# Optimization experiments

Measured on AMD Instinct MI355X. Metric: run time of the kernel, lower is better.

Reference implementation:

```python
import jax, jax.numpy as jnp
import numpy as np

EPS = 1e-8

def squash(t, axis=-1):
    sq = jnp.sum(t * t, axis=axis, keepdims=True)
    scale = sq / (1.0 + sq)
    return scale * t / jnp.sqrt(sq + EPS)

def setup_inputs() -> dict:
    key = jax.random.key(0)
    k1, k2 = jax.random.split(key)
    B, N_IN, D_IN, N_OUT, D_OUT = 256, 1152, 8, 10, 16
    x = jax.random.normal(k1, (B, N_IN, D_IN), dtype=jnp.float32)
    W = 0.01 * jax.random.normal(k2, (1, N_IN, N_OUT, D_OUT, D_IN), dtype=jnp.float32)
    return {"x": x, "W": W}

def reference(x, W):
    # u_hat[b,n,o,j] = sum_i W[0,n,o,j,i] * x[b,n,i]   -> (B, N_in, N_out, D_out)
    u_hat = jnp.einsum('noji,bni->bnoj', W[0], x)
    # b_ij starts with batch dim 1 (as in original torch code) and broadcasts
    b_ij = jnp.zeros((1, u_hat.shape[1], u_hat.shape[2], 1), dtype=u_hat.dtype)
    v_j = None
    for _ in range(3):  # fixed 3 routing iterations
        c_ij = jax.nn.softmax(b_ij, axis=2)            # over output capsules
        s_j = jnp.sum(c_ij * u_hat, axis=1, keepdims=True)  # (B,1,N_out,D_out)
        v_j = squash(s_j, axis=-1)
        b_ij = b_ij + jnp.sum(u_hat * v_j, axis=-1, keepdims=True)
    return jnp.squeeze(v_j, axis=1)  # (B, N_out, D_out)
```

## Files before the change

kernel.cpp:

```cpp
#include <hip/hip_runtime.h>

#define B_ 256
#define N_IN 1152
#define N_OUT 10
#define D_OUT 16
#define OJ 160
#define SN (B_*OJ)
#define LOG2E 1.44269504088896340736f
#define NPB 16
#define NPW 4
#define NSG (N_IN/NPB)
#define NPASSB (NSG*16)
#define NPB1 32
#define NSG1 (N_IN/NPB1)

typedef __attribute__((ext_vector_type(8))) short bf16x8;
typedef __attribute__((ext_vector_type(4))) float f32x4;

#define NW_ELEMS (N_IN*N_OUT*D_OUT)
#define NX_ELEMS (B_*N_IN)
#define NWB (NW_ELEMS/256)
#define NTILES ((N_IN/16)*(B_/16))

__device__ __forceinline__ unsigned short f2bf(float f) {
  unsigned u = __float_as_uint(f);
  u += 0x7fffu + ((u >> 16) & 1u);
  return (unsigned short)(u >> 16);
}
__device__ __forceinline__ float bf2f(unsigned short s) {
  return __uint_as_float(((unsigned)s) << 16);
}
__device__ __forceinline__ void split8(const float* p, bf16x8& vh, bf16x8& vl) {
  const float4 a = *(const float4*)p;
  const float4 b = *(const float4*)(p + 4);
  const float w[8] = {a.x,a.y,a.z,a.w,b.x,b.y,b.z,b.w};
#pragma unroll
  for (int e=0;e<8;e++){
    unsigned short hh = f2bf(w[e]);
    vh[e] = (short)hh;
    vl[e] = (short)f2bf(w[e] - bf2f(hh));
  }
}

template<int CTRL>
__device__ __forceinline__ float dpp_add(float xx) {
  int y = __builtin_amdgcn_mov_dpp(__float_as_int(xx), CTRL, 0xF, 0xF, false);
  return xx + __int_as_float(y);
}
__device__ __forceinline__ float quad_sum4(float xx) {
  xx = dpp_add<0xB1>(xx);
  xx = dpp_add<0x4E>(xx);
  return xx;
}

__device__ __forceinline__ void sgbg_map(int bid, int& sg, int& bg) {
  const int xcd = bid & 7, q = bid >> 3;
  sg = xcd*9 + (q % 9);
  bg = q / 9;
}

__global__ __launch_bounds__(256) void pack_all(const float* __restrict__ W,
                                                const float* __restrict__ x,
                                                short* __restrict__ WH, short* __restrict__ WL,
                                                short* __restrict__ XH, short* __restrict__ XL) {
  const int bid = blockIdx.x, tid = threadIdx.x;
  if (bid < NWB) {
    const int t = bid*256 + tid;
    bf16x8 vh, vl; split8(W + (size_t)t*8, vh, vl);
    ((bf16x8*)WH)[t] = vh; ((bf16x8*)WL)[t] = vl;
  } else {
    __shared__ bf16x8 TH[16*17], TL[16*17];
    const int tile = bid - NWB;
    const int nt = tile >> 4, bt = tile & 15;
    const int nn = tid & 15, bb = tid >> 4;
    bf16x8 vh, vl;
    split8(x + ((size_t)(bt*16+bb)*N_IN + nt*16+nn)*8, vh, vl);
    TH[nn*17 + bb] = vh; TL[nn*17 + bb] = vl;
    __syncthreads();
    const int bb2 = tid & 15, nn2 = tid >> 4;
    const size_t o = (size_t)(nt*16+nn2)*B_ + bt*16 + bb2;
    ((bf16x8*)XH)[o] = TH[nn2*17 + bb2];
    ((bf16x8*)XL)[o] = TL[nn2*17 + bb2];
  }
}

__global__ __launch_bounds__(256) void caps_pass1(const short* __restrict__ WH,
                                                  const short* __restrict__ XH,
                                                  float* __restrict__ P) {
  __shared__ f32x4 red[3*640];
  const int tid = threadIdx.x, w = tid >> 6, l = tid & 63;
  const int bb = l & 15, c = l >> 4;
  const int sg = blockIdx.x, bg = blockIdx.y;
  const int b0 = bg * 16;
  const int n0 = sg*NPB1 + w*8;

  f32x4 acc[N_OUT];
  const f32x4 zz = {0.f,0.f,0.f,0.f};
#pragma unroll
  for (int o=0;o<N_OUT;o++) acc[o] = zz;

#pragma unroll
  for (int grp=0; grp<2; ++grp) {
    const int nb = n0 + grp*4 + c;
    const bf16x8 bfrag = *(const bf16x8*)&XH[((size_t)nb*B_ + b0 + bb)*8];
    const short* Ap = &WH[(size_t)nb*1280 + bb*8];
#pragma unroll
    for (int o=0;o<N_OUT;o++) {
      const bf16x8 afrag = *(const bf16x8*)&Ap[o*128];
      acc[o] = __builtin_amdgcn_mfma_f32_16x16x32_bf16(afrag, bfrag, acc[o], 0,0,0);
    }
  }

  if (w) {
#pragma unroll
    for (int o=0;o<N_OUT;o++) red[(w-1)*640 + o*64 + l] = acc[o];
  }
  __syncthreads();
  if (!w) {
    float* Pp = &P[(size_t)sg*SN + (size_t)(b0 + bb)*OJ + c*4];
#pragma unroll
    for (int o=0;o<N_OUT;o++) {
      acc[o] += red[o*64+l] + red[640+o*64+l] + red[1280+o*64+l];
      *(f32x4*)&Pp[o*16] = acc[o];
    }
  }
}

__global__ __launch_bounds__(256) void caps_pass23(const short* __restrict__ WH,
                                                   const short* __restrict__ WL,
                                                   const short* __restrict__ XH,
                                                   const short* __restrict__ XL,
                                                   const float* __restrict__ veff,
                                                   float* __restrict__ P) {
  __shared__ f32x4 red[3*640];
  int sg, bg; sgbg_map(blockIdx.x, sg, bg);
  const int tid = threadIdx.x, w = tid >> 6, l = tid & 63;
  const int bb = l & 15, c = l >> 4;
  const int b0 = bg * 16;
  const int n0 = sg * NPB + w * NPW;
  const short* Abase = (c & 1)  ? WL : WH;
  const short* Bbase = (c >> 1) ? XL : XH;

  f32x4 vj[N_OUT], acc[N_OUT];
  const f32x4 zz = {0.f,0.f,0.f,0.f};
  const float* vp = &veff[(size_t)(b0+bb)*OJ + c*4];
#pragma unroll
  for (int o=0;o<N_OUT;o++) { vj[o] = *(const f32x4*)&vp[o*16]; acc[o] = zz; }

  for (int nn=0; nn<NPW; ++nn) {
    const int n = n0 + nn;
    const bf16x8 bfrag = *(const bf16x8*)&Bbase[((size_t)n*B_ + b0 + bb)*8];
    const short* Ap = &Abase[(size_t)n*1280 + bb*8];
    f32x4 u[N_OUT];
#pragma unroll
    for (int o=0;o<N_OUT;o++) {
      const bf16x8 afrag = *(const bf16x8*)&Ap[o*128];
      u[o] = __builtin_amdgcn_mfma_f32_16x16x32_bf16(afrag, bfrag, zz, 0,0,0);
    }
    float ez[N_OUT], Z = 0.f;
#pragma unroll
    for (int o=0;o<N_OUT;o++) {
      float t = u[o][0]*vj[o][0] + u[o][1]*vj[o][1]
              + u[o][2]*vj[o][2] + u[o][3]*vj[o][3];
      t += __shfl_xor(t, 16);
      t += __shfl_xor(t, 32);
      ez[o] = exp2f(t);
      Z += ez[o];
    }
    const float invZ = __builtin_amdgcn_rcpf(Z);
#pragma unroll
    for (int o=0;o<N_OUT;o++) acc[o] += (ez[o] * invZ) * u[o];
  }

  if (w) {
#pragma unroll
    for (int o=0;o<N_OUT;o++) red[(w-1)*640 + o*64 + l] = acc[o];
  }
  __syncthreads();
  if (!w) {
    float* Pp = &P[(size_t)sg*SN + (size_t)(b0 + bb)*OJ + c*4];
#pragma unroll
    for (int o=0;o<N_OUT;o++) {
      acc[o] += red[o*64+l] + red[640+o*64+l] + red[1280+o*64+l];
      *(f32x4*)&Pp[o*16] = acc[o];
    }
  }
}

template<int GC>
__global__ __launch_bounds__(256) void caps_finish(const float* __restrict__ P, float scale,
                                                   const float* __restrict__ vprev,
                                                   float* __restrict__ vout, float lscale) {
  const int e0 = (blockIdx.x*256 + threadIdx.x)*4;
  f32x4 t = {0.f,0.f,0.f,0.f};
#pragma unroll 8
  for (int g=0; g<GC; ++g) t += *(const f32x4*)&P[(size_t)g*SN + e0];
  t *= scale;
  const float sq = quad_sum4(t[0]*t[0] + t[1]*t[1] + t[2]*t[2] + t[3]*t[3]);
  const float k = (sq/(1.f+sq)) * rsqrtf(sq + 1e-8f) * lscale;
  f32x4 v = t * k;
  if (vprev != nullptr) v += *(const f32x4*)&vprev[e0];
  *(f32x4*)&vout[e0] = v;
}

extern "C" void kernel_launch(void* const* d_in, const int* in_sizes, int n_in,
                              void* d_out, int out_size, void* d_ws, size_t ws_size,
                              hipStream_t stream) {
  const float* x = (const float*)d_in[0];
  const float* W = (const float*)d_in[1];
  float* out = (float*)d_out;

  float* P   = (float*)d_ws;
  float* v1  = P  + (size_t)NSG*SN;
  float* v12 = v1 + SN;
  short* WH = (short*)(v12 + SN);
  short* WL = WH + (size_t)NW_ELEMS*8;
  short* XH = WL + (size_t)NW_ELEMS*8;
  short* XL = XH + (size_t)NX_ELEMS*8;

  pack_all<<<NWB + NTILES, 256, 0, stream>>>(W, x, WH, WL, XH, XL);

  caps_pass1<<<dim3(NSG1,16), 256, 0, stream>>>(WH, XH, P);
  caps_finish<NSG1><<<SN/1024, 256, 0, stream>>>(P, 0.1f, nullptr, v1, LOG2E);

  caps_pass23<<<NPASSB, 256, 0, stream>>>(WH, WL, XH, XL, v1, P);
  caps_finish<NSG><<<SN/1024, 256, 0, stream>>>(P, 1.0f, v1, v12, LOG2E);

  caps_pass23<<<NPASSB, 256, 0, stream>>>(WH, WL, XH, XL, v12, P);
  caps_finish<NSG><<<SN/1024, 256, 0, stream>>>(P, 1.0f, nullptr, out, 1.0f);
}
```

Measured before the change: 79.44 us.

## Fuse first routing pass into pack kernel, converting fp32 inputs to bf16 on the fly

The separate pack and pass-1 kernels are merged into one launch. Pass-1 blocks now read fp32 W and x directly and convert them to bf16 with v_cvt_pk_bf16_f32, so they no longer wait for the packed buffers. This removes one kernel launch and the serial dependency between packing and the first pass. In exchange, pass-1 reads W and x twice from global memory and uses the hardware conversion's rounding rather than the software round-to-nearest-even.

```diff
diff --git a/kernel.cpp b/kernel.cpp
--- a/kernel.cpp
+++ b/kernel.cpp
@@ -13,6 +13,7 @@
 #define NPASSB (NSG*16)
 #define NPB1 32
 #define NSG1 (N_IN/NPB1)
+#define NP1B (NSG1*16)
 
 typedef __attribute__((ext_vector_type(8))) short bf16x8;
 typedef __attribute__((ext_vector_type(4))) float f32x4;
@@ -42,6 +43,17 @@
   }
 }
 
+__device__ __forceinline__ bf16x8 cvt8(const float* p) {
+  const f32x4 a = *(const f32x4*)p;
+  const f32x4 b = *(const f32x4*)(p + 4);
+  union { unsigned u[4]; bf16x8 v; } r;
+  asm("v_cvt_pk_bf16_f32 %0, %1, %2" : "=v"(r.u[0]) : "v"(a[0]), "v"(a[1]));
+  asm("v_cvt_pk_bf16_f32 %0, %1, %2" : "=v"(r.u[1]) : "v"(a[2]), "v"(a[3]));
+  asm("v_cvt_pk_bf16_f32 %0, %1, %2" : "=v"(r.u[2]) : "v"(b[0]), "v"(b[1]));
+  asm("v_cvt_pk_bf16_f32 %0, %1, %2" : "=v"(r.u[3]) : "v"(b[2]), "v"(b[3]));
+  return r.v;
+}
+
 template<int CTRL>
 __device__ __forceinline__ float dpp_add(float xx) {
   int y = __builtin_amdgcn_mov_dpp(__float_as_int(xx), CTRL, 0xF, 0xF, false);
@@ -59,18 +71,59 @@
   bg = q / 9;
 }
 
-__global__ __launch_bounds__(256) void pack_all(const float* __restrict__ W,
-                                                const float* __restrict__ x,
-                                                short* __restrict__ WH, short* __restrict__ WL,
-                                                short* __restrict__ XH, short* __restrict__ XL) {
+__global__ __launch_bounds__(256) void d1_all(
+    const float* __restrict__ W, const float* __restrict__ x,
+    short* __restrict__ WH, short* __restrict__ WL,
+    short* __restrict__ XH, short* __restrict__ XL,
+    float* __restrict__ P) {
+  __shared__ f32x4 red[3*640];
   const int bid = blockIdx.x, tid = threadIdx.x;
-  if (bid < NWB) {
-    const int t = bid*256 + tid;
+
+  if (bid < NP1B) {
+    const int sg = bid >> 4, bg = bid & 15;
+    const int w = tid >> 6, l = tid & 63;
+    const int bb = l & 15, c = l >> 4;
+    const int b0 = bg * 16;
+    const int n0 = sg*NPB1 + w*8;
+
+    f32x4 acc[N_OUT];
+    const f32x4 zz = {0.f,0.f,0.f,0.f};
+#pragma unroll
+    for (int o=0;o<N_OUT;o++) acc[o] = zz;
+
+#pragma unroll
+    for (int grp=0; grp<2; ++grp) {
+      const int nb = n0 + grp*4 + c;
+      const bf16x8 bfrag = cvt8(&x[((size_t)(b0+bb)*N_IN + nb)*8]);
+      const float* Wp = &W[(size_t)nb*1280 + bb*8];
+#pragma unroll
+      for (int o=0;o<N_OUT;o++) {
+        const bf16x8 afrag = cvt8(Wp + o*128);
+        acc[o] = __builtin_amdgcn_mfma_f32_16x16x32_bf16(afrag, bfrag, acc[o], 0,0,0);
+      }
+    }
+
+    if (w) {
+#pragma unroll
+      for (int o=0;o<N_OUT;o++) red[(w-1)*640 + o*64 + l] = acc[o];
+    }
+    __syncthreads();
+    if (!w) {
+      float* Pp = &P[(size_t)sg*SN + (size_t)(b0 + bb)*OJ + c*4];
+#pragma unroll
+      for (int o=0;o<N_OUT;o++) {
+        acc[o] += red[o*64+l] + red[640+o*64+l] + red[1280+o*64+l];
+        *(f32x4*)&Pp[o*16] = acc[o];
+      }
+    }
+  } else if (bid < NP1B + NWB) {
+    const int t = (bid - NP1B)*256 + tid;
     bf16x8 vh, vl; split8(W + (size_t)t*8, vh, vl);
     ((bf16x8*)WH)[t] = vh; ((bf16x8*)WL)[t] = vl;
   } else {
-    __shared__ bf16x8 TH[16*17], TL[16*17];
-    const int tile = bid - NWB;
+    bf16x8* TH = (bf16x8*)red;
+    bf16x8* TL = TH + 272;
+    const int tile = bid - NP1B - NWB;
     const int nt = tile >> 4, bt = tile & 15;
     const int nn = tid & 15, bb = tid >> 4;
     bf16x8 vh, vl;
@@ -81,48 +134,6 @@
     const size_t o = (size_t)(nt*16+nn2)*B_ + bt*16 + bb2;
     ((bf16x8*)XH)[o] = TH[nn2*17 + bb2];
     ((bf16x8*)XL)[o] = TL[nn2*17 + bb2];
-  }
-}
-
-__global__ __launch_bounds__(256) void caps_pass1(const short* __restrict__ WH,
-                                                  const short* __restrict__ XH,
-                                                  float* __restrict__ P) {
-  __shared__ f32x4 red[3*640];
-  const int tid = threadIdx.x, w = tid >> 6, l = tid & 63;
-  const int bb = l & 15, c = l >> 4;
-  const int sg = blockIdx.x, bg = blockIdx.y;
-  const int b0 = bg * 16;
-  const int n0 = sg*NPB1 + w*8;
-
-  f32x4 acc[N_OUT];
-  const f32x4 zz = {0.f,0.f,0.f,0.f};
-#pragma unroll
-  for (int o=0;o<N_OUT;o++) acc[o] = zz;
-
-#pragma unroll
-  for (int grp=0; grp<2; ++grp) {
-    const int nb = n0 + grp*4 + c;
-    const bf16x8 bfrag = *(const bf16x8*)&XH[((size_t)nb*B_ + b0 + bb)*8];
-    const short* Ap = &WH[(size_t)nb*1280 + bb*8];
-#pragma unroll
-    for (int o=0;o<N_OUT;o++) {
-      const bf16x8 afrag = *(const bf16x8*)&Ap[o*128];
-      acc[o] = __builtin_amdgcn_mfma_f32_16x16x32_bf16(afrag, bfrag, acc[o], 0,0,0);
-    }
-  }
-
-  if (w) {
-#pragma unroll
-    for (int o=0;o<N_OUT;o++) red[(w-1)*640 + o*64 + l] = acc[o];
-  }
-  __syncthreads();
-  if (!w) {
-    float* Pp = &P[(size_t)sg*SN + (size_t)(b0 + bb)*OJ + c*4];
-#pragma unroll
-    for (int o=0;o<N_OUT;o++) {
-      acc[o] += red[o*64+l] + red[640+o*64+l] + red[1280+o*64+l];
-      *(f32x4*)&Pp[o*16] = acc[o];
-    }
   }
 }
 
@@ -218,14 +229,10 @@
   short* XH = WL + (size_t)NW_ELEMS*8;
   short* XL = XH + (size_t)NX_ELEMS*8;
 
-  pack_all<<<NWB + NTILES, 256, 0, stream>>>(W, x, WH, WL, XH, XL);
-
-  caps_pass1<<<dim3(NSG1,16), 256, 0, stream>>>(WH, XH, P);
+  d1_all<<<NP1B + NWB + NTILES, 256, 0, stream>>>(W, x, WH, WL, XH, XL, P);
   caps_finish<NSG1><<<SN/1024, 256, 0, stream>>>(P, 0.1f, nullptr, v1, LOG2E);
-
   caps_pass23<<<NPASSB, 256, 0, stream>>>(WH, WL, XH, XL, v1, P);
   caps_finish<NSG><<<SN/1024, 256, 0, stream>>>(P, 1.0f, v1, v12, LOG2E);
-
   caps_pass23<<<NPASSB, 256, 0, stream>>>(WH, WL, XH, XL, v12, P);
   caps_finish<NSG><<<SN/1024, 256, 0, stream>>>(P, 1.0f, nullptr, out, 1.0f);
 }
```

After: 80.99 us. No clear change (+2.0%).
